# Performance work log

Measured on AMD Instinct MI355X. Metric: run time of the kernel, lower is better.

## Reference

```python
import jax, jax.numpy as jnp
import numpy as np

N, E, D, H = 50000, 300000, 256, 2
C = D // H  # per-head out_channels (PyG TransformerConv, concat=True)
LN_EPS = 1e-5


def setup_inputs() -> dict:
    key = jax.random.key(0)
    ks = jax.random.split(key, 10)
    s = 1.0 / np.sqrt(D).astype(np.float32)
    return {
        "x": jax.random.normal(ks[0], (N, D), jnp.float32),
        "edge_attr": jax.random.normal(ks[1], (E, D), jnp.float32),
        "edge_index": jax.random.randint(ks[2], (2, E), 0, N, dtype=jnp.int32),
        "Wq": jax.random.normal(ks[3], (D, D), jnp.float32) * s,
        "bq": jnp.zeros((D,), jnp.float32),
        "Wk": jax.random.normal(ks[4], (D, D), jnp.float32) * s,
        "bk": jnp.zeros((D,), jnp.float32),
        "Wv": jax.random.normal(ks[5], (D, D), jnp.float32) * s,
        "bv": jnp.zeros((D,), jnp.float32),
        "We": jax.random.normal(ks[6], (D, D), jnp.float32) * s,  # lin_edge, bias=False in PyG
        "Wskip": jax.random.normal(ks[7], (D, D), jnp.float32) * s,
        "bskip": jnp.zeros((D,), jnp.float32),
        "ln_gamma": jnp.ones((D,), jnp.float32),
        "ln_beta": jnp.zeros((D,), jnp.float32),
    }


def reference(x, edge_attr, edge_index, Wq, bq, Wk, bk, Wv, bv, We,
              Wskip, bskip, ln_gamma, ln_beta):
    src, dst = edge_index[0], edge_index[1]  # message flows src(j) -> dst(i)

    # node-level projections (dense GEMMs), reshaped to [*, H, C]
    q = (x @ Wq + bq).reshape(N, H, C)
    k = (x @ Wk + bk).reshape(N, H, C)
    v = (x @ Wv + bv).reshape(N, H, C)
    e = (edge_attr @ We).reshape(E, H, C)

    # per-edge gather; edge features added to both key and value (PyG TransformerConv)
    k_e = k[src] + e            # [E, H, C]
    v_e = v[src] + e            # [E, H, C]

    # attention logits per edge/head, scaled by sqrt(C)
    alpha = jnp.einsum('ehc,ehc->eh', q[dst], k_e) / np.sqrt(C).astype(np.float32)

    # segment softmax over incoming edges of each destination node
    amax = jax.ops.segment_max(alpha, dst, num_segments=N)   # [N, H]
    ex = jnp.exp(alpha - amax[dst])                          # [E, H]
    denom = jax.ops.segment_sum(ex, dst, num_segments=N)     # [N, H]
    w = ex / (denom[dst] + 1e-16)                            # [E, H]

    # weighted scatter-add aggregation, concat heads
    agg = jax.ops.segment_sum(w[:, :, None] * v_e, dst, num_segments=N)
    out = agg.reshape(N, D)

    # root/skip connection (root_weight=True, beta=False)
    out = out + x @ Wskip + bskip

    # LayerNorm + ReLU
    mu = out.mean(-1, keepdims=True)
    var = out.var(-1, keepdims=True)
    out = (out - mu) * jax.lax.rsqrt(var + LN_EPS) * ln_gamma + ln_beta
    return jax.nn.relu(out)
```

## Files before the change

kernel.cpp:

```cpp
#include <hip/hip_runtime.h>
#include <hip/hip_bf16.h>

#define N_NODES 50000
#define N_EDGES 300000
#define CPAD 53248

typedef __attribute__((ext_vector_type(4))) float f32x4;
typedef __attribute__((ext_vector_type(4))) int i32x4;
typedef __attribute__((ext_vector_type(8))) __bf16 bf16x8;
typedef __attribute__((ext_vector_type(4))) __bf16 bf16x4;

#define GLDS16(g, l)                                                                   \
    __builtin_amdgcn_global_load_lds((const __attribute__((address_space(1))) void*)(g), \
                                     (__attribute__((address_space(3))) void*)(l), 16, 0, 0)

#define CBAR(N)                                                              \
    do {                                                                     \
        asm volatile("s_waitcnt vmcnt(" #N ") lgkmcnt(0)" ::: "memory");     \
        __builtin_amdgcn_s_barrier();                                        \
        __builtin_amdgcn_sched_barrier(0);                                   \
    } while (0)

__global__ void prep_kernel(const float* __restrict__ Wq, const float* __restrict__ bq,
                            const float* __restrict__ Wk, const float* __restrict__ bk,
                            const float* __restrict__ Wv, const float* __restrict__ bv,
                            const float* __restrict__ Wskip, const float* __restrict__ bskip,
                            const float* __restrict__ We,
                            __bf16* __restrict__ Wp, float* __restrict__ bias_p,
                            __bf16* __restrict__ Wes, int* __restrict__ counts) {
    int b = blockIdx.x;
    if (b >= 1280) {
        counts[(b - 1280) * 256 + threadIdx.x] = 0;
        return;
    }
    int idx = b * 256 + threadIdx.x;
    if (idx < 1024 * 256) {
        int k = idx >> 10, n = idx & 1023;
        int nb = n >> 8, nn = n & 255;
        const float* W = nb == 0 ? Wq : nb == 1 ? Wk : nb == 2 ? Wv : Wskip;
        int step = k >> 5, kg = (k >> 3) & 3, j = k & 7;
        Wp[nb * 65536 + step * 8192 + (kg * 256 + nn) * 8 + j] = (__bf16)W[k * 256 + nn];
        if (k == 0) {
            const float* bb = nb == 0 ? bq : nb == 1 ? bk : nb == 2 ? bv : bskip;
            bias_p[n] = bb[nn];
        }
    } else {
        int r = idx - 1024 * 256;
        int k = r >> 8, n = r & 255;
        int step = k >> 5, kg = (k >> 3) & 3, j = k & 7;
        Wes[step * 8192 + (kg * 256 + n) * 8 + j] = (__bf16)We[k * 256 + n];
    }
}

__global__ void count_kernel(const int* __restrict__ dst, int* __restrict__ counts) {
    int i = blockIdx.x * 256 + threadIdx.x;
    if (i < N_EDGES) atomicAdd(&counts[dst[i]], 1);
}

__global__ __launch_bounds__(1024) void scan_kernel(const int* __restrict__ counts,
                                                    int* __restrict__ row_ptr,
                                                    int* __restrict__ cursor) {
    int tid = threadIdx.x;
    int base = tid * 52;
    int loc[52];
    int s = 0;
#pragma unroll
    for (int j = 0; j < 13; j++) {
        i32x4 v = *reinterpret_cast<const i32x4*>(counts + base + j * 4);
        loc[j * 4 + 0] = v.x; loc[j * 4 + 1] = v.y;
        loc[j * 4 + 2] = v.z; loc[j * 4 + 3] = v.w;
        s += v.x + v.y + v.z + v.w;
    }
    __shared__ int buf[1024];
    buf[tid] = s;
    __syncthreads();
    for (int off = 1; off < 1024; off <<= 1) {
        int t = (tid >= off) ? buf[tid - off] : 0;
        __syncthreads();
        buf[tid] += t;
        __syncthreads();
    }
    int run = buf[tid] - s;
#pragma unroll
    for (int j = 0; j < 52; j++) {
        int idx = base + j;
        if (idx < N_NODES) {
            row_ptr[idx] = run;
            cursor[idx] = run;
            run += loc[j];
        } else if (idx == N_NODES) {
            row_ptr[N_NODES] = run;
        }
    }
}

__global__ void scatter_kernel(const int* __restrict__ src, const int* __restrict__ dst,
                               int* __restrict__ cursor, int* __restrict__ cidx,
                               int* __restrict__ sperm) {
    int i = blockIdx.x * 256 + threadIdx.x;
    if (i < N_EDGES) {
        int p = atomicAdd(&cursor[dst[i]], 1);
        cidx[p] = i;
        sperm[p] = src[i];
    }
}

__global__ __launch_bounds__(512, 4) void gemm_kernel(
    const float* __restrict__ xA, const __bf16* __restrict__ Wp,
    const float* __restrict__ bias_p, __bf16* __restrict__ proj,
    const float* __restrict__ eA, const __bf16* __restrict__ Wes,
    __bf16* __restrict__ e_out, int nodeBlocks) {
    __shared__ __bf16 As[2][128 * 32];
    __shared__ __bf16 Bs[3][256 * 32];
    int tid = threadIdx.x;

    const float* A; int M, Nout, m0, nb;
    const __bf16* Wsw; const float* bias; __bf16* C;
    if ((int)blockIdx.x < nodeBlocks) {
        int t = blockIdx.x;
        nb = t & 3; m0 = (t >> 2) * 128;
        A = xA; M = N_NODES; Nout = 1024;
        Wsw = Wp; bias = bias_p; C = proj;
    } else {
        int t = blockIdx.x - nodeBlocks;
        nb = 0; m0 = t * 128;
        A = eA; M = N_EDGES; Nout = 256;
        Wsw = Wes; bias = nullptr; C = e_out;
    }
    const __bf16* Bbase = Wsw + (size_t)nb * 65536;

    int lane = tid & 63, w = tid >> 6;
    int wr = w >> 2, wc = w & 3;
    int l15 = lane & 15, kg4 = lane >> 4;

    f32x4 acc[4][4];
#pragma unroll
    for (int r = 0; r < 4; r++)
#pragma unroll
        for (int c = 0; c < 4; c++) acc[r][c] = (f32x4)0.f;

    int arow = tid >> 2, akg = tid & 3;
    int schunk = akg * 128 + (arow ^ (akg << 1));
    bool aok = (m0 + arow) < M;
    const float* Aptr = A + (size_t)(aok ? (m0 + arow) : 0) * 256 + akg * 8;

    f32x4 a0 = aok ? *reinterpret_cast<const f32x4*>(Aptr) : (f32x4)0.f;
    f32x4 a1 = aok ? *reinterpret_cast<const f32x4*>(Aptr + 4) : (f32x4)0.f;
    GLDS16(Bbase + (size_t)tid * 8, &Bs[0][w * 64 * 8]);
    GLDS16(Bbase + (size_t)(tid + 512) * 8, &Bs[0][(512 + w * 64) * 8]);
    GLDS16(Bbase + (size_t)(8192 + tid * 8), &Bs[1][w * 64 * 8]);
    GLDS16(Bbase + (size_t)(8192 + (tid + 512) * 8), &Bs[1][(512 + w * 64) * 8]);
    {
        bf16x8 ab;
        ab[0] = (__bf16)a0.x; ab[1] = (__bf16)a0.y; ab[2] = (__bf16)a0.z; ab[3] = (__bf16)a0.w;
        ab[4] = (__bf16)a1.x; ab[5] = (__bf16)a1.y; ab[6] = (__bf16)a1.z; ab[7] = (__bf16)a1.w;
        *reinterpret_cast<bf16x8*>(&As[0][schunk * 8]) = ab;
    }
    CBAR(2);

#pragma unroll
    for (int t = 0; t < 8; ++t) {
        if (t < 7) {
            int k0 = (t + 1) * 32;
            a0 = aok ? *reinterpret_cast<const f32x4*>(Aptr + k0) : (f32x4)0.f;
            a1 = aok ? *reinterpret_cast<const f32x4*>(Aptr + k0 + 4) : (f32x4)0.f;
        }
        if (t < 6) {
            GLDS16(Bbase + (size_t)((t + 2) * 8192 + tid * 8), &Bs[(t + 2) % 3][w * 64 * 8]);
            GLDS16(Bbase + (size_t)((t + 2) * 8192 + (tid + 512) * 8),
                   &Bs[(t + 2) % 3][(512 + w * 64) * 8]);
        }
        bf16x8 af[4], bfr[4];
#pragma unroll
        for (int r = 0; r < 4; r++)
            af[r] = *reinterpret_cast<const bf16x8*>(
                &As[t & 1][(kg4 * 128 + ((wr * 64 + r * 16 + l15) ^ (kg4 << 1))) * 8]);
#pragma unroll
        for (int c = 0; c < 4; c++)
            bfr[c] = *reinterpret_cast<const bf16x8*>(
                &Bs[t % 3][(kg4 * 256 + wc * 64 + c * 16 + l15) * 8]);
#pragma unroll
        for (int r = 0; r < 4; r++)
#pragma unroll
            for (int c = 0; c < 4; c++)
                acc[r][c] = __builtin_amdgcn_mfma_f32_16x16x32_bf16(af[r], bfr[c], acc[r][c], 0, 0, 0);
        if (t < 7) {
            bf16x8 ab;
            ab[0] = (__bf16)a0.x; ab[1] = (__bf16)a0.y; ab[2] = (__bf16)a0.z; ab[3] = (__bf16)a0.w;
            ab[4] = (__bf16)a1.x; ab[5] = (__bf16)a1.y; ab[6] = (__bf16)a1.z; ab[7] = (__bf16)a1.w;
            *reinterpret_cast<bf16x8*>(&As[(t + 1) & 1][schunk * 8]) = ab;
        }
        CBAR(2);
    }

#pragma unroll
    for (int r = 0; r < 4; r++) {
        int growb = m0 + wr * 64 + r * 16 + kg4 * 4;
#pragma unroll
        for (int i2 = 0; i2 < 4; i2++) {
            int grow = growb + i2;
            if (grow < M) {
#pragma unroll
                for (int c = 0; c < 4; c++) {
                    int lcol = wc * 64 + c * 16 + l15;
                    float v = acc[r][c][i2];
                    if (bias) v += bias[nb * 256 + lcol];
                    C[(size_t)grow * Nout + nb * 256 + lcol] = (__bf16)v;
                }
            }
        }
    }
}

__global__ __launch_bounds__(256) void attn_kernel(const __bf16* __restrict__ proj,
                                                   const __bf16* __restrict__ e_out,
                                                   const int* __restrict__ cidx,
                                                   const int* __restrict__ sperm,
                                                   const int* __restrict__ row_ptr,
                                                   const float* __restrict__ gamma,
                                                   const float* __restrict__ beta,
                                                   float* __restrict__ out) {
    int w = threadIdx.x >> 6, lane = threadIdx.x & 63;
    int d = blockIdx.x * 4 + w;
    if (d >= N_NODES) return;
    const float rscale = 0.08838834764831845f;

    bf16x4 qb = *reinterpret_cast<const bf16x4*>(proj + (size_t)d * 1024 + lane * 4);
    float q0 = (float)qb.x * rscale, q1 = (float)qb.y * rscale;
    float q2 = (float)qb.z * rscale, q3 = (float)qb.w * rscale;
    int start = row_ptr[d], end = row_ptr[d + 1];

    float den = 0.f;
    f32x4 acc = (f32x4)0.f;
    int i = start;
    int n4 = start + ((end - start) & ~3);
    for (; i < n4; i += 4) {
        int sA[4], eI[4];
#pragma unroll
        for (int j = 0; j < 4; j++) {
            sA[j] = sperm[i + j];
            eI[j] = cidx[i + j];
        }
        bf16x4 kA[4], vA[4], eE[4];
#pragma unroll
        for (int j = 0; j < 4; j++) {
            const __bf16* pr = proj + (size_t)sA[j] * 1024 + 256 + lane * 4;
            kA[j] = *reinterpret_cast<const bf16x4*>(pr);
            vA[j] = *reinterpret_cast<const bf16x4*>(pr + 256);
            eE[j] = *reinterpret_cast<const bf16x4*>(e_out + (size_t)eI[j] * 256 + lane * 4);
        }
        float p[4];
#pragma unroll
        for (int j = 0; j < 4; j++)
            p[j] = q0 * ((float)kA[j].x + (float)eE[j].x) + q1 * ((float)kA[j].y + (float)eE[j].y) +
                   q2 * ((float)kA[j].z + (float)eE[j].z) + q3 * ((float)kA[j].w + (float)eE[j].w);
#pragma unroll
        for (int o = 16; o > 0; o >>= 1) {
#pragma unroll
            for (int j = 0; j < 4; j++) p[j] += __shfl_xor(p[j], o, 32);
        }
#pragma unroll
        for (int j = 0; j < 4; j++) {
            float wj = __expf(p[j]);
            den += wj;
            acc.x += wj * ((float)vA[j].x + (float)eE[j].x);
            acc.y += wj * ((float)vA[j].y + (float)eE[j].y);
            acc.z += wj * ((float)vA[j].z + (float)eE[j].z);
            acc.w += wj * ((float)vA[j].w + (float)eE[j].w);
        }
    }
    for (; i < end; ++i) {
        int s0 = sperm[i];
        int e0i = cidx[i];
        const __bf16* pr = proj + (size_t)s0 * 1024 + 256 + lane * 4;
        bf16x4 k0 = *reinterpret_cast<const bf16x4*>(pr);
        bf16x4 v0 = *reinterpret_cast<const bf16x4*>(pr + 256);
        bf16x4 e0 = *reinterpret_cast<const bf16x4*>(e_out + (size_t)e0i * 256 + lane * 4);
        float p = q0 * ((float)k0.x + (float)e0.x) + q1 * ((float)k0.y + (float)e0.y) +
                  q2 * ((float)k0.z + (float)e0.z) + q3 * ((float)k0.w + (float)e0.w);
#pragma unroll
        for (int o = 16; o > 0; o >>= 1) p += __shfl_xor(p, o, 32);
        float wj = __expf(p);
        den += wj;
        acc.x += wj * ((float)v0.x + (float)e0.x);
        acc.y += wj * ((float)v0.y + (float)e0.y);
        acc.z += wj * ((float)v0.z + (float)e0.z);
        acc.w += wj * ((float)v0.w + (float)e0.w);
    }

    float inv = 1.f / (den + 1e-16f);
    bf16x4 skb = *reinterpret_cast<const bf16x4*>(proj + (size_t)d * 1024 + 768 + lane * 4);
    f32x4 o;
    o.x = acc.x * inv + (float)skb.x;
    o.y = acc.y * inv + (float)skb.y;
    o.z = acc.z * inv + (float)skb.z;
    o.w = acc.w * inv + (float)skb.w;

    float s1 = o.x + o.y + o.z + o.w;
    float s2 = o.x * o.x + o.y * o.y + o.z * o.z + o.w * o.w;
#pragma unroll
    for (int off = 32; off > 0; off >>= 1) {
        s1 += __shfl_xor(s1, off, 64);
        s2 += __shfl_xor(s2, off, 64);
    }
    float mean = s1 * (1.f / 256.f);
    float var = s2 * (1.f / 256.f) - mean * mean;
    float rstd = rsqrtf(var + 1e-5f);
    f32x4 g = *reinterpret_cast<const f32x4*>(gamma + lane * 4);
    f32x4 b = *reinterpret_cast<const f32x4*>(beta + lane * 4);
    o.x = fmaxf(0.f, (o.x - mean) * rstd * g.x + b.x);
    o.y = fmaxf(0.f, (o.y - mean) * rstd * g.y + b.y);
    o.z = fmaxf(0.f, (o.z - mean) * rstd * g.z + b.z);
    o.w = fmaxf(0.f, (o.w - mean) * rstd * g.w + b.w);
    *reinterpret_cast<f32x4*>(out + (size_t)d * 256 + lane * 4) = o;
}

extern "C" void kernel_launch(void* const* d_in, const int* in_sizes, int n_in,
                              void* d_out, int out_size, void* d_ws, size_t ws_size,
                              hipStream_t stream) {
    const float* x = (const float*)d_in[0];
    const float* edge_attr = (const float*)d_in[1];
    const int* edge_index = (const int*)d_in[2];
    const float* Wq = (const float*)d_in[3];
    const float* bq = (const float*)d_in[4];
    const float* Wk = (const float*)d_in[5];
    const float* bk = (const float*)d_in[6];
    const float* Wv = (const float*)d_in[7];
    const float* bv = (const float*)d_in[8];
    const float* We = (const float*)d_in[9];
    const float* Wskip = (const float*)d_in[10];
    const float* bskip = (const float*)d_in[11];
    const float* gamma = (const float*)d_in[12];
    const float* beta = (const float*)d_in[13];
    float* out = (float*)d_out;
    const int* src = edge_index;
    const int* dst = edge_index + N_EDGES;

    char* ws = (char*)d_ws;
    size_t off = 0;
    auto alloc = [&](size_t bytes) {
        size_t p = off;
        off += (bytes + 255) & ~(size_t)255;
        return p;
    };
    __bf16* proj = (__bf16*)(ws + alloc((size_t)N_NODES * 1024 * 2));
    __bf16* e_out = (__bf16*)(ws + alloc((size_t)N_EDGES * 256 * 2));
    __bf16* Wp = (__bf16*)(ws + alloc(1024 * 256 * 2));
    __bf16* Wes = (__bf16*)(ws + alloc(256 * 256 * 2));
    float* bias_p = (float*)(ws + alloc(1024 * 4));
    int* row_ptr = (int*)(ws + alloc((N_NODES + 1) * 4));
    int* cursor = (int*)(ws + alloc(N_NODES * 4));
    int* counts = (int*)(ws + alloc(CPAD * 4));
    int* cidx = (int*)(ws + alloc(N_EDGES * 4));
    int* sperm = (int*)(ws + alloc(N_EDGES * 4));

    int nodeBlocks = ((N_NODES + 127) / 128) * 4;
    int edgeBlocks = (N_EDGES + 127) / 128;

    prep_kernel<<<1488, 256, 0, stream>>>(Wq, bq, Wk, bk, Wv, bv, Wskip, bskip, We,
                                          Wp, bias_p, Wes, counts);
    count_kernel<<<(N_EDGES + 255) / 256, 256, 0, stream>>>(dst, counts);
    scan_kernel<<<1, 1024, 0, stream>>>(counts, row_ptr, cursor);
    scatter_kernel<<<(N_EDGES + 255) / 256, 256, 0, stream>>>(src, dst, cursor, cidx, sperm);
    gemm_kernel<<<nodeBlocks + edgeBlocks, 512, 0, stream>>>(
        x, Wp, bias_p, proj, edge_attr, Wes, e_out, nodeBlocks);
    attn_kernel<<<(N_NODES + 3) / 4, 256, 0, stream>>>(proj, e_out, cidx, sperm, row_ptr,
                                                       gamma, beta, out);
}
```

Baseline: 407.8 us.

## Halve GEMM M-tile and load A fragments directly from global into registers

The GEMM tile height drops from 128 to 64 rows, and the shared-memory staging buffer for A is removed. Each wave now loads its own fp32 A rows straight into registers with a two-deep register prefetch, converts them to bf16 there, and feeds the MFMAs directly. Barrier wait counts are adjusted to the new number of outstanding loads. This removes LDS traffic for A and the A store/read, and frees LDS and registers for occupancy. In exchange, B tiles are reused over fewer rows, so B loads per output double and the grid doubles.

```diff
diff --git a/kernel.cpp b/kernel.cpp
--- a/kernel.cpp
+++ b/kernel.cpp
@@ -110,7 +110,6 @@
     const float* __restrict__ bias_p, __bf16* __restrict__ proj,
     const float* __restrict__ eA, const __bf16* __restrict__ Wes,
     __bf16* __restrict__ e_out, int nodeBlocks) {
-    __shared__ __bf16 As[2][128 * 32];
     __shared__ __bf16 Bs[3][256 * 32];
     int tid = threadIdx.x;
 
@@ -118,12 +117,12 @@
     const __bf16* Wsw; const float* bias; __bf16* C;
     if ((int)blockIdx.x < nodeBlocks) {
         int t = blockIdx.x;
-        nb = t & 3; m0 = (t >> 2) * 128;
+        nb = t & 3; m0 = (t >> 2) * 64;
         A = xA; M = N_NODES; Nout = 1024;
         Wsw = Wp; bias = bias_p; C = proj;
     } else {
         int t = blockIdx.x - nodeBlocks;
-        nb = 0; m0 = t * 128;
+        nb = 0; m0 = t * 64;
         A = eA; M = N_EDGES; Nout = 256;
         Wsw = Wes; bias = nullptr; C = e_out;
     }
@@ -133,69 +132,70 @@
     int wr = w >> 2, wc = w & 3;
     int l15 = lane & 15, kg4 = lane >> 4;
 
-    f32x4 acc[4][4];
-#pragma unroll
-    for (int r = 0; r < 4; r++)
+    f32x4 acc[2][4];
+#pragma unroll
+    for (int r = 0; r < 2; r++)
 #pragma unroll
         for (int c = 0; c < 4; c++) acc[r][c] = (f32x4)0.f;
 
-    int arow = tid >> 2, akg = tid & 3;
-    int schunk = akg * 128 + (arow ^ (akg << 1));
-    bool aok = (m0 + arow) < M;
-    const float* Aptr = A + (size_t)(aok ? (m0 + arow) : 0) * 256 + akg * 8;
-
-    f32x4 a0 = aok ? *reinterpret_cast<const f32x4*>(Aptr) : (f32x4)0.f;
-    f32x4 a1 = aok ? *reinterpret_cast<const f32x4*>(Aptr + 4) : (f32x4)0.f;
+    int row0 = m0 + wr * 32 + l15;
+    int row1 = row0 + 16;
+    const float* Ar0 = A + (size_t)(row0 < M ? row0 : 0) * 256 + kg4 * 8;
+    const float* Ar1 = A + (size_t)(row1 < M ? row1 : 0) * 256 + kg4 * 8;
+
     GLDS16(Bbase + (size_t)tid * 8, &Bs[0][w * 64 * 8]);
     GLDS16(Bbase + (size_t)(tid + 512) * 8, &Bs[0][(512 + w * 64) * 8]);
     GLDS16(Bbase + (size_t)(8192 + tid * 8), &Bs[1][w * 64 * 8]);
     GLDS16(Bbase + (size_t)(8192 + (tid + 512) * 8), &Bs[1][(512 + w * 64) * 8]);
-    {
-        bf16x8 ab;
-        ab[0] = (__bf16)a0.x; ab[1] = (__bf16)a0.y; ab[2] = (__bf16)a0.z; ab[3] = (__bf16)a0.w;
-        ab[4] = (__bf16)a1.x; ab[5] = (__bf16)a1.y; ab[6] = (__bf16)a1.z; ab[7] = (__bf16)a1.w;
-        *reinterpret_cast<bf16x8*>(&As[0][schunk * 8]) = ab;
-    }
-    CBAR(2);
+    f32x4 ar[2][4];
+    ar[0][0] = *reinterpret_cast<const f32x4*>(Ar0);
+    ar[0][1] = *reinterpret_cast<const f32x4*>(Ar0 + 4);
+    ar[0][2] = *reinterpret_cast<const f32x4*>(Ar1);
+    ar[0][3] = *reinterpret_cast<const f32x4*>(Ar1 + 4);
+    ar[1][0] = *reinterpret_cast<const f32x4*>(Ar0 + 32);
+    ar[1][1] = *reinterpret_cast<const f32x4*>(Ar0 + 36);
+    ar[1][2] = *reinterpret_cast<const f32x4*>(Ar1 + 32);
+    ar[1][3] = *reinterpret_cast<const f32x4*>(Ar1 + 36);
+    CBAR(10);
 
 #pragma unroll
     for (int t = 0; t < 8; ++t) {
-        if (t < 7) {
-            int k0 = (t + 1) * 32;
-            a0 = aok ? *reinterpret_cast<const f32x4*>(Aptr + k0) : (f32x4)0.f;
-            a1 = aok ? *reinterpret_cast<const f32x4*>(Aptr + k0 + 4) : (f32x4)0.f;
+        bf16x8 af[2];
+#pragma unroll
+        for (int r = 0; r < 2; r++) {
+            f32x4 lo = ar[t & 1][r * 2], hi = ar[t & 1][r * 2 + 1];
+            bf16x8 ab;
+            ab[0] = (__bf16)lo.x; ab[1] = (__bf16)lo.y; ab[2] = (__bf16)lo.z; ab[3] = (__bf16)lo.w;
+            ab[4] = (__bf16)hi.x; ab[5] = (__bf16)hi.y; ab[6] = (__bf16)hi.z; ab[7] = (__bf16)hi.w;
+            af[r] = ab;
         }
         if (t < 6) {
             GLDS16(Bbase + (size_t)((t + 2) * 8192 + tid * 8), &Bs[(t + 2) % 3][w * 64 * 8]);
             GLDS16(Bbase + (size_t)((t + 2) * 8192 + (tid + 512) * 8),
                    &Bs[(t + 2) % 3][(512 + w * 64) * 8]);
-        }
-        bf16x8 af[4], bfr[4];
-#pragma unroll
-        for (int r = 0; r < 4; r++)
-            af[r] = *reinterpret_cast<const bf16x8*>(
-                &As[t & 1][(kg4 * 128 + ((wr * 64 + r * 16 + l15) ^ (kg4 << 1))) * 8]);
+            int k0 = (t + 2) * 32;
+            ar[t & 1][0] = *reinterpret_cast<const f32x4*>(Ar0 + k0);
+            ar[t & 1][1] = *reinterpret_cast<const f32x4*>(Ar0 + k0 + 4);
+            ar[t & 1][2] = *reinterpret_cast<const f32x4*>(Ar1 + k0);
+            ar[t & 1][3] = *reinterpret_cast<const f32x4*>(Ar1 + k0 + 4);
+        }
+        bf16x8 bfr[4];
 #pragma unroll
         for (int c = 0; c < 4; c++)
             bfr[c] = *reinterpret_cast<const bf16x8*>(
                 &Bs[t % 3][(kg4 * 256 + wc * 64 + c * 16 + l15) * 8]);
 #pragma unroll
-        for (int r = 0; r < 4; r++)
+        for (int r = 0; r < 2; r++)
 #pragma unroll
             for (int c = 0; c < 4; c++)
                 acc[r][c] = __builtin_amdgcn_mfma_f32_16x16x32_bf16(af[r], bfr[c], acc[r][c], 0, 0, 0);
-        if (t < 7) {
-            bf16x8 ab;
-            ab[0] = (__bf16)a0.x; ab[1] = (__bf16)a0.y; ab[2] = (__bf16)a0.z; ab[3] = (__bf16)a0.w;
-            ab[4] = (__bf16)a1.x; ab[5] = (__bf16)a1.y; ab[6] = (__bf16)a1.z; ab[7] = (__bf16)a1.w;
-            *reinterpret_cast<bf16x8*>(&As[(t + 1) & 1][schunk * 8]) = ab;
-        }
-        CBAR(2);
-    }
-
-#pragma unroll
-    for (int r = 0; r < 4; r++) {
-        int growb = m0 + wr * 64 + r * 16 + kg4 * 4;
+        if (t < 6) CBAR(10);
+        else if (t == 6) CBAR(4);
+    }
+
+#pragma unroll
+    for (int r = 0; r < 2; r++) {
+        int growb = m0 + wr * 32 + r * 16 + kg4 * 4;
 #pragma unroll
         for (int i2 = 0; i2 < 4; i2++) {
             int grow = growb + i2;
@@ -354,8 +354,8 @@
     int* cidx = (int*)(ws + alloc(N_EDGES * 4));
     int* sperm = (int*)(ws + alloc(N_EDGES * 4));
 
-    int nodeBlocks = ((N_NODES + 127) / 128) * 4;
-    int edgeBlocks = (N_EDGES + 127) / 128;
+    int nodeBlocks = ((N_NODES + 63) / 64) * 4;
+    int edgeBlocks = (N_EDGES + 63) / 64;
 
     prep_kernel<<<1488, 256, 0, stream>>>(Wq, bq, Wk, bk, Wv, bv, Wskip, bskip, We,
                                           Wp, bias_p, Wes, counts);
```

Measured after the change: 517.4 us. +26.9%, slower.
